# Performance work log

Hardware: AMD Instinct MI355X
Metric: run time of the kernel (lower is better)

## Reference

```python
import jax, jax.numpy as jnp
import numpy as np

K = 512   # codebook entries per group (num_embeddings // 4)
D = 128   # dim per group (embedding_dim // 4)
BETA = 0.25


def setup_inputs() -> dict:
    key = jax.random.key(0)
    k0, k1, k2, k3, k4 = jax.random.split(key, 5)
    latents = jax.random.normal(k0, (16, 2048, 512), dtype=jnp.float32)
    scale = 1.0 / K
    w1 = jax.random.uniform(k1, (K, D), dtype=jnp.float32, minval=-scale, maxval=scale)
    w2 = jax.random.uniform(k2, (K, D), dtype=jnp.float32, minval=-scale, maxval=scale)
    w3 = jax.random.uniform(k3, (K, D), dtype=jnp.float32, minval=-scale, maxval=scale)
    w4 = jax.random.uniform(k4, (K, D), dtype=jnp.float32, minval=-scale, maxval=scale)
    return {"latents": latents, "w1": w1, "w2": w2, "w3": w3, "w4": w4}


def _vq(latents, w1, w2, w3, w4):
    B, S, E = latents.shape
    # Slicing [:, :, g*D:(g+1)*D] is equivalent to reshape into groups.
    x = latents.reshape(B, S, 4, D)                    # [B,S,4,D]
    W = jnp.stack([w1, w2, w3, w4], axis=0)            # [4,K,D]
    x_sq = jnp.sum(x * x, axis=-1, keepdims=True)      # [B,S,4,1]
    w_sq = jnp.sum(W * W, axis=-1)                     # [4,K]
    cross = jnp.einsum('bsgd,gkd->bsgk', x, W)         # [B,S,4,K]
    dist = x_sq + w_sq[None, None, :, :] - 2.0 * cross
    idx = jnp.argmin(dist, axis=-1)                    # [B,S,4]
    g_idx = jnp.arange(4)[None, None, :]
    q = W[g_idx, idx]                                  # [B,S,4,D]
    # per-group MSE losses (mean over B,S,D)
    sg = jax.lax.stop_gradient
    commit = jnp.mean((sg(q) - x) ** 2, axis=(0, 1, 3))   # [4]
    embed = jnp.mean((q - sg(x)) ** 2, axis=(0, 1, 3))    # [4]
    vq_loss = jnp.sum(BETA * commit + embed)
    # straight-through estimator
    q_st = x + sg(q - x)
    return q_st.reshape(B, S, E), vq_loss


def reference(latents, w1, w2, w3, w4):
    return _vq(latents, w1, w2, w3, w4)
```

## Files before the change

### kernel.cpp

```cpp
#include <hip/hip_runtime.h>
#include <stdint.h>

typedef __attribute__((ext_vector_type(8))) short short8;
typedef __attribute__((ext_vector_type(4))) float f32x4;

#define BIG 4.0f

static __device__ __forceinline__ short f2bf(float f) {
    union { float f; uint32_t u; } v; v.f = f;
    uint32_t u = v.u;
    return (short)((u + 0x7FFFu + ((u >> 16) & 1u)) >> 16);
}

static __device__ __forceinline__ void gload_lds16(const void* g, void* l) {
    __builtin_amdgcn_global_load_lds(
        (const __attribute__((address_space(1))) unsigned int*)g,
        (__attribute__((address_space(3))) unsigned int*)l, 16, 0, 0);
}


__global__ void vq_prep_kernel(const float* __restrict__ w0, const float* __restrict__ w1,
                               const float* __restrict__ w2, const float* __restrict__ w3,
                               float* __restrict__ ws) {
    int tid = blockIdx.x * blockDim.x + threadIdx.x;
    const float* wg = (tid < 512) ? w0 : (tid < 1024) ? w1 : (tid < 1536) ? w2 : w3;
    int c  = tid & 511;
    int g  = tid >> 9;
    int nt = c >> 4, lr = c & 15;
    const float* src = wg + (size_t)c * 128;
    char* cb = (char*)ws + 65536 + (size_t)g * 131072;
    float s = 0.f;
    #pragma unroll
    for (int cg = 0; cg < 16; cg++) {
        int ks = cg >> 2, lh = cg & 3;
        float4 v0 = *(const float4*)(src + cg * 8);
        float4 v1 = *(const float4*)(src + cg * 8 + 4);
        s += v0.x*v0.x + v0.y*v0.y + v0.z*v0.z + v0.w*v0.w
           + v1.x*v1.x + v1.y*v1.y + v1.z*v1.z + v1.w*v1.w;
        short8 b;
        b[0] = f2bf(v0.x); b[1] = f2bf(v0.y); b[2] = f2bf(v0.z); b[3] = f2bf(v0.w);
        b[4] = f2bf(v1.x); b[5] = f2bf(v1.y); b[6] = f2bf(v1.z); b[7] = f2bf(v1.w);
        *(short8*)(cb + ((size_t)((nt * 4 + ks) * 64 + lh * 16 + lr) * 16)) = b;
    }
    ws[64 + tid] = BIG - 0.5f * s;
}

__global__ __launch_bounds__(256, 2)
void vq_main_kernel(const float* __restrict__ lat,
                    const float* __restrict__ w0, const float* __restrict__ w1,
                    const float* __restrict__ w2, const float* __restrict__ w3,
                    float* __restrict__ out, float* __restrict__ ws) {
    __shared__ __align__(16) short lw[32768];
    __shared__ float lwsq[512];
    __shared__ float slsum[4];

    const int bid   = blockIdx.x;
    const int g     = bid >> 7;
    const int tbase = (bid & 127) * 256;
    const float* wg = (g == 0) ? w0 : (g == 1) ? w1 : (g == 2) ? w2 : w3;
    const char* cbg = (const char*)ws + 65536 + (size_t)g * 131072;

    const int t    = threadIdx.x;
    const int wave = t >> 6;
    const int l    = t & 63;
    const int lr   = l & 15;
    const int lh   = l >> 4;
    const uint32_t invlr = 511 - lr;

    lwsq[t]       = ws[64 + g * 512 + t];
    lwsq[t + 256] = ws[64 + g * 512 + t + 256];

    {
        const char* gsrc = cbg + wave * 16384 + l * 16;
        char* ldst = (char*)lw + wave * 16384;
        #pragma unroll
        for (int j = 0; j < 16; j++)
            gload_lds16(gsrc + j * 1024, ldst + j * 1024);
    }

    short8 afrag[4][4];
    float  xsq[4];
    const int wtok = tbase + wave * 64;
    #pragma unroll
    for (int mt = 0; mt < 4; mt++) {
        int token = wtok + mt * 16 + lr;
        const float* xp = lat + (size_t)token * 512 + g * 128 + lh * 8;
        float part = 0.f;
        #pragma unroll
        for (int ks = 0; ks < 4; ks++) {
            float4 v0 = *(const float4*)(xp + ks * 32);
            float4 v1 = *(const float4*)(xp + ks * 32 + 4);
            part += v0.x*v0.x + v0.y*v0.y + v0.z*v0.z + v0.w*v0.w
                  + v1.x*v1.x + v1.y*v1.y + v1.z*v1.z + v1.w*v1.w;
            short8 a;
            a[0] = f2bf(v0.x); a[1] = f2bf(v0.y); a[2] = f2bf(v0.z); a[3] = f2bf(v0.w);
            a[4] = f2bf(v1.x); a[5] = f2bf(v1.y); a[6] = f2bf(v1.z); a[7] = f2bf(v1.w);
            afrag[mt][ks] = a;
        }
        part += __shfl_xor(part, 16);
        part += __shfl_xor(part, 32);
        xsq[mt] = part;
    }

    uint32_t runkey[16];
    #pragma unroll
    for (int i = 0; i < 16; i++) runkey[i] = 0u;

    const char* lwb = (const char*)lw + l * 16;

    #pragma unroll
    for (int h = 0; h < 2; h++) {
        __syncthreads();

        short8 bf[2][4];
        float  hv[2];
        #pragma unroll
        for (int p = 0; p < 2; p++) {
            const char* base = lwb + p * 4096;
            bf[p][0] = *(const short8*)(base);
            bf[p][1] = *(const short8*)(base + 1024);
            bf[p][2] = *(const short8*)(base + 2048);
            bf[p][3] = *(const short8*)(base + 3072);
            hv[p] = lwsq[(h * 16 + p) * 16 + lr];
        }

        #pragma unroll 2
        for (int nt = 0; nt < 16; nt++) {
            const int cur = nt & 1;
            short8 c0 = bf[cur][0], c1 = bf[cur][1], c2 = bf[cur][2], c3 = bf[cur][3];
            float  hn = hv[cur];
            {
                const char* nbase = lwb + ((nt + 2) & 15) * 4096;
                bf[cur][0] = *(const short8*)(nbase);
                bf[cur][1] = *(const short8*)(nbase + 1024);
                bf[cur][2] = *(const short8*)(nbase + 2048);
                bf[cur][3] = *(const short8*)(nbase + 3072);
                hv[cur] = lwsq[(h * 16 + ((nt + 2) & 15)) * 16 + lr];
            }
            const uint32_t invc = invlr - (uint32_t)((h * 16 + nt) * 16);
            #pragma unroll
            for (int mt = 0; mt < 4; mt++) {
                f32x4 acc = {hn, hn, hn, hn};
                acc = __builtin_amdgcn_mfma_f32_16x16x32_bf16(afrag[mt][0], c0, acc, 0, 0, 0);
                acc = __builtin_amdgcn_mfma_f32_16x16x32_bf16(afrag[mt][1], c1, acc, 0, 0, 0);
                acc = __builtin_amdgcn_mfma_f32_16x16x32_bf16(afrag[mt][2], c2, acc, 0, 0, 0);
                acc = __builtin_amdgcn_mfma_f32_16x16x32_bf16(afrag[mt][3], c3, acc, 0, 0, 0);
                #pragma unroll
                for (int r = 0; r < 4; r++) {
                    uint32_t key = (__float_as_uint(acc[r]) & 0xFFFFFE00u) | invc;
                    int i = mt * 4 + r;
                    runkey[i] = max(runkey[i], key);
                }
            }
        }

        if (h == 0) {
            __syncthreads();
            const char* gsrc = cbg + 65536 + wave * 16384 + l * 16;
            char* ldst = (char*)lw + wave * 16384;
            #pragma unroll
            for (int j = 0; j < 16; j++)
                gload_lds16(gsrc + j * 1024, ldst + j * 1024);
        }
    }

    #pragma unroll
    for (int i = 0; i < 16; i++) {
        uint32_t k = runkey[i];
        k = max(k, (uint32_t)__shfl_xor((int)k, 1));
        k = max(k, (uint32_t)__shfl_xor((int)k, 2));
        k = max(k, (uint32_t)__shfl_xor((int)k, 4));
        k = max(k, (uint32_t)__shfl_xor((int)k, 8));
        runkey[i] = k;
    }

    int runidx[16];
    float lsum = 0.f;
    #pragma unroll
    for (int mt = 0; mt < 4; mt++) {
        #pragma unroll
        for (int r = 0; r < 4; r++) {
            int i = mt * 4 + r;
            uint32_t k = runkey[i];
            runidx[i] = 511 - (int)(k & 0x1FFu);
            float val = __uint_as_float(k & 0xFFFFFE00u);
            int row = lh * 4 + r;
            float xs = __shfl(xsq[mt], (l & 48) | row);
            if (lr == 0) lsum += xs + 2.f * BIG - 2.f * val;
        }
    }
    lsum += __shfl_xor(lsum, 16);
    lsum += __shfl_xor(lsum, 32);
    if (l == 0) slsum[wave] = lsum;
    __syncthreads();
    if (t == 0) ws[4096 + bid] = slsum[0] + slsum[1] + slsum[2] + slsum[3];

    #pragma unroll
    for (int it = 0; it < 32; it++) {
        const int j0 = it * 2, j1 = it * 2 + 1;
        int idx0 = __shfl(runidx[((j0 >> 4) << 2) | (j0 & 3)], ((j0 >> 2) & 3) << 4);
        int idx1 = __shfl(runidx[((j1 >> 4) << 2) | (j1 & 3)], ((j1 >> 2) & 3) << 4);
        int idx  = (l >= 32) ? idx1 : idx0;
        int tloc = it * 2 + (l >> 5);
        int col  = (l & 31) * 4;
        float4 v = *(const float4*)(wg + (size_t)idx * 128 + col);
        *(float4*)(out + (size_t)(wtok + tloc) * 512 + g * 128 + col) = v;
    }
}

__global__ void vq_finalize_kernel(const float* __restrict__ ws, float* __restrict__ out) {
    __shared__ float s8[8];
    float v = ws[4096 + threadIdx.x];
    #pragma unroll
    for (int m = 1; m < 64; m <<= 1) v += __shfl_xor(v, m);
    if ((threadIdx.x & 63) == 0) s8[threadIdx.x >> 6] = v;
    __syncthreads();
    if (threadIdx.x == 0) {
        float s = 0.f;
        #pragma unroll
        for (int i = 0; i < 8; i++) s += s8[i];
        out[16777216] = 1.25f * s * (1.0f / 4194304.0f);
    }
}

extern "C" void kernel_launch(void* const* d_in, const int* in_sizes, int n_in,
                              void* d_out, int out_size, void* d_ws, size_t ws_size,
                              hipStream_t stream) {
    const float* lat = (const float*)d_in[0];
    const float* w1  = (const float*)d_in[1];
    const float* w2  = (const float*)d_in[2];
    const float* w3  = (const float*)d_in[3];
    const float* w4  = (const float*)d_in[4];
    float* out = (float*)d_out;
    float* ws  = (float*)d_ws;

    vq_prep_kernel<<<8, 256, 0, stream>>>(w1, w2, w3, w4, ws);
    vq_main_kernel<<<512, 256, 0, stream>>>(lat, w1, w2, w3, w4, out, ws);
    vq_finalize_kernel<<<1, 512, 0, stream>>>(ws, out);
}
```

Measured before the change: 47.55 us.

## Split gather into separate kernel, widen prep parallelism, fold finalize into gather

The fused score+gather kernel is split. The score kernel now writes packed 16-bit argmin indices to workspace, and a new gather kernel with 1024 blocks and higher occupancy copies codebook rows to the output. The loss finalize reduction moves into block 0 of the gather kernel, so one launch is dropped. The prep kernel now uses 16 threads per code with a shuffle reduction instead of one thread per code, spreading its work over 128 blocks. The cost is an extra round trip for the indices through global memory, and the gather can no longer overlap with scoring inside one kernel.

```diff
diff --git a/kernel.cpp b/kernel.cpp
--- a/kernel.cpp
+++ b/kernel.cpp
@@ -22,42 +22,38 @@
 __global__ void vq_prep_kernel(const float* __restrict__ w0, const float* __restrict__ w1,
                                const float* __restrict__ w2, const float* __restrict__ w3,
                                float* __restrict__ ws) {
-    int tid = blockIdx.x * blockDim.x + threadIdx.x;
-    const float* wg = (tid < 512) ? w0 : (tid < 1024) ? w1 : (tid < 1536) ? w2 : w3;
-    int c  = tid & 511;
-    int g  = tid >> 9;
-    int nt = c >> 4, lr = c & 15;
-    const float* src = wg + (size_t)c * 128;
+    int tid = blockIdx.x * 256 + threadIdx.x;
+    int code = tid >> 4;
+    int u    = tid & 15;
+    int g = code >> 9, c = code & 511;
+    int nt = c >> 4, lr = c & 15, ks = u >> 2, lh = u & 3;
+    const float* wg = (g == 0) ? w0 : (g == 1) ? w1 : (g == 2) ? w2 : w3;
+    const float* src = wg + (size_t)c * 128 + u * 8;
+    float4 v0 = *(const float4*)(src);
+    float4 v1 = *(const float4*)(src + 4);
+    float s = v0.x*v0.x + v0.y*v0.y + v0.z*v0.z + v0.w*v0.w
+            + v1.x*v1.x + v1.y*v1.y + v1.z*v1.z + v1.w*v1.w;
+    short8 b;
+    b[0] = f2bf(v0.x); b[1] = f2bf(v0.y); b[2] = f2bf(v0.z); b[3] = f2bf(v0.w);
+    b[4] = f2bf(v1.x); b[5] = f2bf(v1.y); b[6] = f2bf(v1.z); b[7] = f2bf(v1.w);
     char* cb = (char*)ws + 65536 + (size_t)g * 131072;
-    float s = 0.f;
-    #pragma unroll
-    for (int cg = 0; cg < 16; cg++) {
-        int ks = cg >> 2, lh = cg & 3;
-        float4 v0 = *(const float4*)(src + cg * 8);
-        float4 v1 = *(const float4*)(src + cg * 8 + 4);
-        s += v0.x*v0.x + v0.y*v0.y + v0.z*v0.z + v0.w*v0.w
-           + v1.x*v1.x + v1.y*v1.y + v1.z*v1.z + v1.w*v1.w;
-        short8 b;
-        b[0] = f2bf(v0.x); b[1] = f2bf(v0.y); b[2] = f2bf(v0.z); b[3] = f2bf(v0.w);
-        b[4] = f2bf(v1.x); b[5] = f2bf(v1.y); b[6] = f2bf(v1.z); b[7] = f2bf(v1.w);
-        *(short8*)(cb + ((size_t)((nt * 4 + ks) * 64 + lh * 16 + lr) * 16)) = b;
-    }
-    ws[64 + tid] = BIG - 0.5f * s;
+    *(short8*)(cb + (size_t)(((nt * 4 + ks) * 64 + lh * 16 + lr) * 16)) = b;
+    s += __shfl_xor(s, 1); s += __shfl_xor(s, 2);
+    s += __shfl_xor(s, 4); s += __shfl_xor(s, 8);
+    if (u == 0) ws[64 + code] = BIG - 0.5f * s;
 }
 
 __global__ __launch_bounds__(256, 2)
-void vq_main_kernel(const float* __restrict__ lat,
-                    const float* __restrict__ w0, const float* __restrict__ w1,
-                    const float* __restrict__ w2, const float* __restrict__ w3,
-                    float* __restrict__ out, float* __restrict__ ws) {
+void vq_score_kernel(const float* __restrict__ lat,
+                     float* __restrict__ ws) {
     __shared__ __align__(16) short lw[32768];
     __shared__ float lwsq[512];
     __shared__ float slsum[4];
+    __shared__ int   sidx[256];
 
     const int bid   = blockIdx.x;
     const int g     = bid >> 7;
     const int tbase = (bid & 127) * 256;
-    const float* wg = (g == 0) ? w0 : (g == 1) ? w1 : (g == 2) ? w2 : w3;
     const char* cbg = (const char*)ws + 65536 + (size_t)g * 131072;
 
     const int t    = threadIdx.x;
@@ -174,7 +170,6 @@
         runkey[i] = k;
     }
 
-    int runidx[16];
     float lsum = 0.f;
     #pragma unroll
     for (int mt = 0; mt < 4; mt++) {
@@ -182,11 +177,13 @@
         for (int r = 0; r < 4; r++) {
             int i = mt * 4 + r;
             uint32_t k = runkey[i];
-            runidx[i] = 511 - (int)(k & 0x1FFu);
-            float val = __uint_as_float(k & 0xFFFFFE00u);
             int row = lh * 4 + r;
             float xs = __shfl(xsq[mt], (l & 48) | row);
-            if (lr == 0) lsum += xs + 2.f * BIG - 2.f * val;
+            if (lr == 0) {
+                float val = __uint_as_float(k & 0xFFFFFE00u);
+                lsum += xs + 2.f * BIG - 2.f * val;
+                sidx[wave * 64 + mt * 16 + row] = 511 - (int)(k & 0x1FFu);
+            }
         }
     }
     lsum += __shfl_xor(lsum, 16);
@@ -195,31 +192,54 @@
     __syncthreads();
     if (t == 0) ws[4096 + bid] = slsum[0] + slsum[1] + slsum[2] + slsum[3];
 
-    #pragma unroll
-    for (int it = 0; it < 32; it++) {
-        const int j0 = it * 2, j1 = it * 2 + 1;
-        int idx0 = __shfl(runidx[((j0 >> 4) << 2) | (j0 & 3)], ((j0 >> 2) & 3) << 4);
-        int idx1 = __shfl(runidx[((j1 >> 4) << 2) | (j1 & 3)], ((j1 >> 2) & 3) << 4);
-        int idx  = (l >= 32) ? idx1 : idx0;
-        int tloc = it * 2 + (l >> 5);
-        int col  = (l & 31) * 4;
+    if (t < 64) {
+        uint32_t u0 = (uint32_t)(sidx[t * 4]     & 0xFFFF) | ((uint32_t)sidx[t * 4 + 1] << 16);
+        uint32_t u1 = (uint32_t)(sidx[t * 4 + 2] & 0xFFFF) | ((uint32_t)sidx[t * 4 + 3] << 16);
+        uint2* gidx = (uint2*)((char*)ws + 655360 + (size_t)(g * 32768 + tbase) * 2);
+        gidx[t] = make_uint2(u0, u1);
+    }
+}
+
+__global__ __launch_bounds__(256, 4)
+void vq_gather_kernel(const float* __restrict__ w0, const float* __restrict__ w1,
+                      const float* __restrict__ w2, const float* __restrict__ w3,
+                      const float* __restrict__ ws, float* __restrict__ out) {
+    __shared__ ushort kidx[128];
+
+    const int b       = blockIdx.x;
+    const int g       = b >> 8;
+    const int tokbase = (b & 255) * 128;
+    const float* wg = (g == 0) ? w0 : (g == 1) ? w1 : (g == 2) ? w2 : w3;
+
+    const int t = threadIdx.x;
+    if (t < 128) {
+        const ushort* idxbuf = (const ushort*)((const char*)ws + 655360)
+                             + g * 32768 + tokbase;
+        kidx[t] = idxbuf[t];
+    }
+    if (b == 0 && t >= 128 && t < 192) {
+        int l2 = t - 128;
+        float v = 0.f;
+        #pragma unroll
+        for (int i = 0; i < 8; i++) v += ws[4096 + l2 * 8 + i];
+        #pragma unroll
+        for (int m = 1; m < 64; m <<= 1) v += __shfl_xor(v, m);
+        if (l2 == 0) out[16777216] = 1.25f * v * (1.0f / 4194304.0f);
+    }
+    __syncthreads();
+
+    const int wave = t >> 6;
+    const int l    = t & 63;
+    const int col  = (l & 31) * 4;
+    const int ub   = wave * 32;
+
+    #pragma unroll 8
+    for (int it = 0; it < 16; it++) {
+        int j0  = ub + it * 2;
+        int idx = (l >= 32) ? kidx[j0 + 1] : kidx[j0];
+        int j   = j0 + (l >> 5);
         float4 v = *(const float4*)(wg + (size_t)idx * 128 + col);
-        *(float4*)(out + (size_t)(wtok + tloc) * 512 + g * 128 + col) = v;
-    }
-}
-
-__global__ void vq_finalize_kernel(const float* __restrict__ ws, float* __restrict__ out) {
-    __shared__ float s8[8];
-    float v = ws[4096 + threadIdx.x];
-    #pragma unroll
-    for (int m = 1; m < 64; m <<= 1) v += __shfl_xor(v, m);
-    if ((threadIdx.x & 63) == 0) s8[threadIdx.x >> 6] = v;
-    __syncthreads();
-    if (threadIdx.x == 0) {
-        float s = 0.f;
-        #pragma unroll
-        for (int i = 0; i < 8; i++) s += s8[i];
-        out[16777216] = 1.25f * s * (1.0f / 4194304.0f);
+        *(float4*)(out + (size_t)(tokbase + j) * 512 + g * 128 + col) = v;
     }
 }
 
@@ -234,7 +254,7 @@
     float* out = (float*)d_out;
     float* ws  = (float*)d_ws;
 
-    vq_prep_kernel<<<8, 256, 0, stream>>>(w1, w2, w3, w4, ws);
-    vq_main_kernel<<<512, 256, 0, stream>>>(lat, w1, w2, w3, w4, out, ws);
-    vq_finalize_kernel<<<1, 512, 0, stream>>>(ws, out);
-}
+    vq_prep_kernel<<<128, 256, 0, stream>>>(w1, w2, w3, w4, ws);
+    vq_score_kernel<<<512, 256, 0, stream>>>(lat, ws);
+    vq_gather_kernel<<<1024, 256, 0, stream>>>(w1, w2, w3, w4, ws, out);
+}
```

After: 48.35 us. About the same (+1.7%).

## Use 512-thread main blocks sharing codebook LDS and parallelize prep per chunk

Applied to the files above, without the earlier changes.

The main kernel now runs 256 blocks of 512 threads (8 waves, 512 tokens each), so each half-codebook staged in LDS serves twice as many tokens. Each wave loads half as much, which cuts global-to-LDS traffic per token, but the grid is smaller and there are fewer blocks per CU. The prep kernel now uses one thread per 8-element chunk with a shuffle reduction for the squared norms, spreading the work over 128 blocks instead of 8. The block loss sum is deferred until after the output gather so one barrier is removed before the stores.

```diff
diff --git a/kernel.cpp b/kernel.cpp
--- a/kernel.cpp
+++ b/kernel.cpp
@@ -22,41 +22,39 @@
 __global__ void vq_prep_kernel(const float* __restrict__ w0, const float* __restrict__ w1,
                                const float* __restrict__ w2, const float* __restrict__ w3,
                                float* __restrict__ ws) {
-    int tid = blockIdx.x * blockDim.x + threadIdx.x;
-    const float* wg = (tid < 512) ? w0 : (tid < 1024) ? w1 : (tid < 1536) ? w2 : w3;
-    int c  = tid & 511;
-    int g  = tid >> 9;
-    int nt = c >> 4, lr = c & 15;
-    const float* src = wg + (size_t)c * 128;
+    int tid = blockIdx.x * 256 + threadIdx.x;
+    int code = tid >> 4;
+    int u    = tid & 15;
+    int g = code >> 9, c = code & 511;
+    int nt = c >> 4, lr = c & 15, ks = u >> 2, lh = u & 3;
+    const float* wg = (g == 0) ? w0 : (g == 1) ? w1 : (g == 2) ? w2 : w3;
+    const float* src = wg + (size_t)c * 128 + u * 8;
+    float4 v0 = *(const float4*)(src);
+    float4 v1 = *(const float4*)(src + 4);
+    float s = v0.x*v0.x + v0.y*v0.y + v0.z*v0.z + v0.w*v0.w
+            + v1.x*v1.x + v1.y*v1.y + v1.z*v1.z + v1.w*v1.w;
+    short8 b;
+    b[0] = f2bf(v0.x); b[1] = f2bf(v0.y); b[2] = f2bf(v0.z); b[3] = f2bf(v0.w);
+    b[4] = f2bf(v1.x); b[5] = f2bf(v1.y); b[6] = f2bf(v1.z); b[7] = f2bf(v1.w);
     char* cb = (char*)ws + 65536 + (size_t)g * 131072;
-    float s = 0.f;
-    #pragma unroll
-    for (int cg = 0; cg < 16; cg++) {
-        int ks = cg >> 2, lh = cg & 3;
-        float4 v0 = *(const float4*)(src + cg * 8);
-        float4 v1 = *(const float4*)(src + cg * 8 + 4);
-        s += v0.x*v0.x + v0.y*v0.y + v0.z*v0.z + v0.w*v0.w
-           + v1.x*v1.x + v1.y*v1.y + v1.z*v1.z + v1.w*v1.w;
-        short8 b;
-        b[0] = f2bf(v0.x); b[1] = f2bf(v0.y); b[2] = f2bf(v0.z); b[3] = f2bf(v0.w);
-        b[4] = f2bf(v1.x); b[5] = f2bf(v1.y); b[6] = f2bf(v1.z); b[7] = f2bf(v1.w);
-        *(short8*)(cb + ((size_t)((nt * 4 + ks) * 64 + lh * 16 + lr) * 16)) = b;
-    }
-    ws[64 + tid] = BIG - 0.5f * s;
-}
-
-__global__ __launch_bounds__(256, 2)
+    *(short8*)(cb + (size_t)(((nt * 4 + ks) * 64 + lh * 16 + lr) * 16)) = b;
+    s += __shfl_xor(s, 1); s += __shfl_xor(s, 2);
+    s += __shfl_xor(s, 4); s += __shfl_xor(s, 8);
+    if (u == 0) ws[64 + code] = BIG - 0.5f * s;
+}
+
+__global__ __launch_bounds__(512, 4)
 void vq_main_kernel(const float* __restrict__ lat,
                     const float* __restrict__ w0, const float* __restrict__ w1,
                     const float* __restrict__ w2, const float* __restrict__ w3,
                     float* __restrict__ out, float* __restrict__ ws) {
     __shared__ __align__(16) short lw[32768];
     __shared__ float lwsq[512];
-    __shared__ float slsum[4];
+    __shared__ float slsum[8];
 
     const int bid   = blockIdx.x;
-    const int g     = bid >> 7;
-    const int tbase = (bid & 127) * 256;
+    const int g     = bid >> 6;
+    const int tbase = (bid & 63) * 512;
     const float* wg = (g == 0) ? w0 : (g == 1) ? w1 : (g == 2) ? w2 : w3;
     const char* cbg = (const char*)ws + 65536 + (size_t)g * 131072;
 
@@ -67,14 +65,13 @@
     const int lh   = l >> 4;
     const uint32_t invlr = 511 - lr;
 
-    lwsq[t]       = ws[64 + g * 512 + t];
-    lwsq[t + 256] = ws[64 + g * 512 + t + 256];
+    lwsq[t] = ws[64 + g * 512 + t];
 
     {
-        const char* gsrc = cbg + wave * 16384 + l * 16;
-        char* ldst = (char*)lw + wave * 16384;
-        #pragma unroll
-        for (int j = 0; j < 16; j++)
+        const char* gsrc = cbg + wave * 8192 + l * 16;
+        char* ldst = (char*)lw + wave * 8192;
+        #pragma unroll
+        for (int j = 0; j < 8; j++)
             gload_lds16(gsrc + j * 1024, ldst + j * 1024);
     }
 
@@ -156,14 +153,15 @@
 
         if (h == 0) {
             __syncthreads();
-            const char* gsrc = cbg + 65536 + wave * 16384 + l * 16;
-            char* ldst = (char*)lw + wave * 16384;
+            const char* gsrc = cbg + 65536 + wave * 8192 + l * 16;
+            char* ldst = (char*)lw + wave * 8192;
             #pragma unroll
-            for (int j = 0; j < 16; j++)
+            for (int j = 0; j < 8; j++)
                 gload_lds16(gsrc + j * 1024, ldst + j * 1024);
         }
     }
 
+    int runidx[16];
     #pragma unroll
     for (int i = 0; i < 16; i++) {
         uint32_t k = runkey[i];
@@ -172,28 +170,23 @@
         k = max(k, (uint32_t)__shfl_xor((int)k, 4));
         k = max(k, (uint32_t)__shfl_xor((int)k, 8));
         runkey[i] = k;
-    }
-
-    int runidx[16];
+        runidx[i] = 511 - (int)(k & 0x1FFu);
+    }
+
     float lsum = 0.f;
     #pragma unroll
     for (int mt = 0; mt < 4; mt++) {
         #pragma unroll
         for (int r = 0; r < 4; r++) {
-            int i = mt * 4 + r;
-            uint32_t k = runkey[i];
-            runidx[i] = 511 - (int)(k & 0x1FFu);
-            float val = __uint_as_float(k & 0xFFFFFE00u);
             int row = lh * 4 + r;
             float xs = __shfl(xsq[mt], (l & 48) | row);
+            float val = __uint_as_float(runkey[mt * 4 + r] & 0xFFFFFE00u);
             if (lr == 0) lsum += xs + 2.f * BIG - 2.f * val;
         }
     }
     lsum += __shfl_xor(lsum, 16);
     lsum += __shfl_xor(lsum, 32);
     if (l == 0) slsum[wave] = lsum;
-    __syncthreads();
-    if (t == 0) ws[4096 + bid] = slsum[0] + slsum[1] + slsum[2] + slsum[3];
 
     #pragma unroll
     for (int it = 0; it < 32; it++) {
@@ -206,21 +199,25 @@
         float4 v = *(const float4*)(wg + (size_t)idx * 128 + col);
         *(float4*)(out + (size_t)(wtok + tloc) * 512 + g * 128 + col) = v;
     }
+
+    __syncthreads();
+    if (t == 0) {
+        float s = 0.f;
+        #pragma unroll
+        for (int i = 0; i < 8; i++) s += slsum[i];
+        ws[4096 + bid] = s;
+    }
 }
 
 __global__ void vq_finalize_kernel(const float* __restrict__ ws, float* __restrict__ out) {
-    __shared__ float s8[8];
+    __shared__ float s4[4];
     float v = ws[4096 + threadIdx.x];
     #pragma unroll
     for (int m = 1; m < 64; m <<= 1) v += __shfl_xor(v, m);
-    if ((threadIdx.x & 63) == 0) s8[threadIdx.x >> 6] = v;
+    if ((threadIdx.x & 63) == 0) s4[threadIdx.x >> 6] = v;
     __syncthreads();
-    if (threadIdx.x == 0) {
-        float s = 0.f;
-        #pragma unroll
-        for (int i = 0; i < 8; i++) s += s8[i];
-        out[16777216] = 1.25f * s * (1.0f / 4194304.0f);
-    }
+    if (threadIdx.x == 0)
+        out[16777216] = 1.25f * (s4[0] + s4[1] + s4[2] + s4[3]) * (1.0f / 4194304.0f);
 }
 
 extern "C" void kernel_launch(void* const* d_in, const int* in_sizes, int n_in,
@@ -234,7 +231,7 @@
     float* out = (float*)d_out;
     float* ws  = (float*)d_ws;
 
-    vq_prep_kernel<<<8, 256, 0, stream>>>(w1, w2, w3, w4, ws);
-    vq_main_kernel<<<512, 256, 0, stream>>>(lat, w1, w2, w3, w4, out, ws);
-    vq_finalize_kernel<<<1, 512, 0, stream>>>(ws, out);
-}
+    vq_prep_kernel<<<128, 256, 0, stream>>>(w1, w2, w3, w4, ws);
+    vq_main_kernel<<<256, 512, 0, stream>>>(lat, w1, w2, w3, w4, out, ws);
+    vq_finalize_kernel<<<1, 256, 0, stream>>>(ws, out);
+}
```

Result: slower. 87.88 us (+84.8%).
